# Kernel optimization log

Measured on AMD Instinct MI355X. Metric: run time of the kernel, lower is better.

## Reference

```python
import jax, jax.numpy as jnp
import numpy as np

B, L, E, H = 4, 2048, 512, 8
D = E // H
FACTOR = 5
U = min(FACTOR * int(np.ceil(np.log(L))), L)  # sample_k == n_top == 40


def setup_inputs() -> dict:
    key0 = jax.random.key(0)
    ks = jax.random.split(key0, 12)
    s = 0.02
    inp = {
        "query": jax.random.normal(ks[0], (B, L, E), jnp.float32),
        "key": jax.random.normal(ks[1], (B, L, E), jnp.float32),
        "value": jax.random.normal(ks[2], (B, L, E), jnp.float32),
        "index_sample": jax.random.randint(ks[3], (L, U), 0, L, jnp.int32),
    }
    for i, nm in enumerate(["q", "k", "v", "o"]):
        inp[f"W{nm}"] = jax.random.normal(ks[4 + i], (E, E), jnp.float32) * s
        inp[f"b{nm}"] = jnp.zeros((E,), jnp.float32)
    return inp


def reference(query, key, value, index_sample, Wq, bq, Wk, bk, Wv, bv, Wo, bo):
    # projections (nn.Linear: x @ W.T + b)
    q = (query @ Wq.T + bq).reshape(B, L, H, D).transpose(0, 2, 1, 3)  # [B,H,L,D]
    k = (key @ Wk.T + bk).reshape(B, L, H, D).transpose(0, 2, 1, 3)
    v = (value @ Wv.T + bv).reshape(B, L, H, D).transpose(0, 2, 1, 3)

    L_Q = L_K = L
    sample_k = index_sample.shape[1]
    n_top = min(sample_k, L_Q)

    # --- _prob_QK: sampled QK scores, note: NO 1/sqrt(D) scaling in source ---
    K_sample = k[:, :, index_sample, :]                      # [B,H,L_Q,sample_k,D]
    QK_sample = jnp.einsum('bhld,bhlsd->bhls', q, K_sample)  # [B,H,L_Q,sample_k]
    M = QK_sample.max(axis=-1) - QK_sample.sum(axis=-1) / L_K
    _, M_top = jax.lax.top_k(M, n_top)                       # [B,H,n_top]
    Q_reduce = jnp.take_along_axis(q, M_top[..., None], axis=2)  # [B,H,n_top,D]
    scores = jnp.einsum('bhud,bhkd->bhuk', Q_reduce, k)      # [B,H,n_top,L_K]

    # --- initial context (eval mode: mean of V) ---
    context = jnp.broadcast_to(v.mean(axis=2, keepdims=True), (B, H, L_Q, D))

    # --- update context at selected queries ---
    attn = jax.nn.softmax(scores, axis=-1)
    upd = jnp.einsum('bhuk,bhkd->bhud', attn, v)             # [B,H,n_top,D]
    bi = jnp.arange(B)[:, None, None]
    hi = jnp.arange(H)[None, :, None]
    context = context.at[bi, hi, M_top].set(upd)

    out = context.transpose(0, 2, 1, 3).reshape(B, L, E) @ Wo.T + bo
    return out
```

## Files before the change

kernel.cpp:

```cpp
#include <hip/hip_runtime.h>
#include <hip/hip_bf16.h>
#include <math.h>

constexpr int BB = 4;
constexpr int LL = 2048;
constexpr int EE = 512;
constexpr int HH = 8;
constexpr int DD = 64;
constexpr int UU = 40;
constexpr int NT = 40;
constexpr int NCH = 32;
constexpr int CK = 64;
constexpr int MVC = 16;
constexpr float NEG_INF = -3.0e38f;

typedef __attribute__((ext_vector_type(8))) short bf8_t;
typedef __attribute__((ext_vector_type(4))) float f4_t;

__device__ __forceinline__ void split2(float x, uint& h, uint& m)
{
    uint  xb = __float_as_uint(x);
    uint  hb = (xb + 0x7fffu + ((xb >> 16) & 1u)) & 0xffff0000u;
    float r  = x - __uint_as_float(hb);
    h = hb >> 16;
    m = (__float_as_uint(r) & 0xffff0000u) >> 16;
}

__device__ __forceinline__ int swz(int row, int c)
{
    return row * 64 + (((c ^ row ^ (row >> 2)) & 3) << 4);
}

__global__ __launch_bounds__(256, 4) void proj_kernel(
    const float* __restrict__ Xq, const float* __restrict__ Xk, const float* __restrict__ Xv,
    const float* __restrict__ Wq, const float* __restrict__ Wk, const float* __restrict__ Wv,
    const float* __restrict__ bq, const float* __restrict__ bk, const float* __restrict__ bv,
    float* __restrict__ Oq, float* __restrict__ Ok, float* __restrict__ Ov)
{
    const float* X; const float* W; const float* bias; float* O;
    if (blockIdx.z == 0)      { X = Xq; W = Wq; bias = bq; O = Oq; }
    else if (blockIdx.z == 1) { X = Xk; W = Wk; bias = bk; O = Ok; }
    else                      { X = Xv; W = Wv; bias = bv; O = Ov; }

    __shared__ char ldsmem[32768];
    char* const LA = ldsmem;
    char* const LB = ldsmem + 16384;

    const int tid  = threadIdx.x;
    const int lane = tid & 63;
    const int wave = tid >> 6;
    const int m0 = blockIdx.y * 128;
    const int n0 = blockIdx.x * 128;

    const int srow  = tid >> 1;
    const int shalf = tid & 1;
    const int w0 = swz(srow, shalf * 2);
    const int w1 = swz(srow, shalf * 2 + 1);
    const float* Aptr = X + (size_t)(m0 + srow) * EE + shalf * 16;
    const float* Bptr = W + (size_t)(n0 + srow) * EE + shalf * 16;

    const int rxor = ((((lane >> 4) ^ lane ^ (lane >> 2)) & 3) << 4);
    const int arow = (wave >> 1) * 64 + (lane & 15);
    const int brow = (wave & 1) * 64 + (lane & 15);

    f4_t acc[4][4];
#pragma unroll
    for (int i = 0; i < 4; i++)
#pragma unroll
        for (int j = 0; j < 4; j++) acc[i][j] = (f4_t)0.0f;

    for (int kt = 0; kt < EE; kt += 32) {
        float fa[16], fb[16];
#pragma unroll
        for (int q = 0; q < 4; q++) {
            *(float4*)(fa + q * 4) = *(const float4*)(Aptr + kt + q * 4);
            *(float4*)(fb + q * 4) = *(const float4*)(Bptr + kt + q * 4);
        }
        uint ahu[8], amu[8], bhu[8], bmu[8];
#pragma unroll
        for (int p = 0; p < 8; p++) {
            uint h0, m0_, h1, m1_;
            split2(fa[2 * p], h0, m0_);
            split2(fa[2 * p + 1], h1, m1_);
            ahu[p] = h0 | (h1 << 16); amu[p] = m0_ | (m1_ << 16);
            split2(fb[2 * p], h0, m0_);
            split2(fb[2 * p + 1], h1, m1_);
            bhu[p] = h0 | (h1 << 16); bmu[p] = m0_ | (m1_ << 16);
        }
        __syncthreads();
        *(uint4*)(LA +     0 + w0) = make_uint4(ahu[0], ahu[1], ahu[2], ahu[3]);
        *(uint4*)(LA +     0 + w1) = make_uint4(ahu[4], ahu[5], ahu[6], ahu[7]);
        *(uint4*)(LA +  8192 + w0) = make_uint4(amu[0], amu[1], amu[2], amu[3]);
        *(uint4*)(LA +  8192 + w1) = make_uint4(amu[4], amu[5], amu[6], amu[7]);
        *(uint4*)(LB +     0 + w0) = make_uint4(bhu[0], bhu[1], bhu[2], bhu[3]);
        *(uint4*)(LB +     0 + w1) = make_uint4(bhu[4], bhu[5], bhu[6], bhu[7]);
        *(uint4*)(LB +  8192 + w0) = make_uint4(bmu[0], bmu[1], bmu[2], bmu[3]);
        *(uint4*)(LB +  8192 + w1) = make_uint4(bmu[4], bmu[5], bmu[6], bmu[7]);
        __syncthreads();

        bf8_t af[4][2];
#pragma unroll
        for (int i = 0; i < 4; i++) {
            const int ro = (arow + i * 16) * 64 + rxor;
            af[i][0] = *(const bf8_t*)(LA +    0 + ro);
            af[i][1] = *(const bf8_t*)(LA + 8192 + ro);
        }
#pragma unroll
        for (int j = 0; j < 4; j++) {
            const int ro = (brow + j * 16) * 64 + rxor;
            bf8_t bh_ = *(const bf8_t*)(LB +    0 + ro);
            bf8_t bm_ = *(const bf8_t*)(LB + 8192 + ro);
#pragma unroll
            for (int i = 0; i < 4; i++) {
                f4_t c = acc[i][j];
                c = __builtin_amdgcn_mfma_f32_16x16x32_bf16(af[i][0], bh_, c, 0, 0, 0);
                c = __builtin_amdgcn_mfma_f32_16x16x32_bf16(af[i][0], bm_, c, 0, 0, 0);
                c = __builtin_amdgcn_mfma_f32_16x16x32_bf16(af[i][1], bh_, c, 0, 0, 0);
                acc[i][j] = c;
            }
        }
    }

#pragma unroll
    for (int j = 0; j < 4; j++) {
        const int n  = n0 + (wave & 1) * 64 + j * 16 + (lane & 15);
        const float bn = bias[n];
        const int h_ = n >> 6, d_ = n & 63;
#pragma unroll
        for (int i = 0; i < 4; i++) {
            const int mb = m0 + (wave >> 1) * 64 + i * 16 + ((lane >> 4) << 2);
#pragma unroll
            for (int r = 0; r < 4; r++) {
                const int m  = mb + r;
                const int b_ = m >> 11;
                const int l_ = m & (LL - 1);
                O[(((size_t)(b_ * HH + h_) * LL + l_) << 6) + d_] = acc[i][j][r] + bn;
            }
        }
    }
}

__global__ __launch_bounds__(256) void meanv_part_kernel(const float* __restrict__ v,
                                                         float* __restrict__ vpart)
{
    const int bh    = blockIdx.x & 31;
    const int chunk = blockIdx.x >> 5;
    const int d  = threadIdx.x & 63;
    const int wv = threadIdx.x >> 6;
    const float* base = v + ((size_t)bh * LL + chunk * 128 + wv * 32) * DD + d;
    float acc = 0.0f;
#pragma unroll
    for (int i = 0; i < 32; i++) acc += base[i * DD];
    __shared__ float red[4][DD];
    red[wv][d] = acc;
    __syncthreads();
    if (wv == 0)
        vpart[(size_t)(chunk * 32 + bh) * DD + d]
            = red[0][d] + red[1][d] + red[2][d] + red[3][d];
}

__global__ __launch_bounds__(64) void meanv_comb_kernel(const float* __restrict__ vpart,
                                                        float* __restrict__ mean_v)
{
    const int bh = blockIdx.x;
    const int d  = threadIdx.x;
    float s = 0.0f;
#pragma unroll
    for (int c = 0; c < MVC; c++) s += vpart[(size_t)(c * 32 + bh) * DD + d];
    mean_v[bh * DD + d] = s * (1.0f / (float)LL);
}

__global__ __launch_bounds__(256) void measure_kernel(const float* __restrict__ q,
                                                      const float* __restrict__ k,
                                                      const int* __restrict__ idx_sample,
                                                      float* __restrict__ M)
{
    int bh   = blockIdx.x & 31;
    int lc   = blockIdx.x >> 5;
    int lane = threadIdx.x & 63;
    int wv   = threadIdx.x >> 6;
    int l    = lc * 4 + wv;
    int s8   = lane >> 3;
    int c    = lane & 7;

    const float* qrow = q + ((size_t)bh * LL + l) * DD + c * 8;
    float4 q0 = *(const float4*)(qrow);
    float4 q1 = *(const float4*)(qrow + 4);

    const float* kbase = k + (size_t)bh * LL * DD;
    const int*   irow  = idx_sample + l * UU;

    float mx = NEG_INF, sum = 0.0f;
#pragma unroll
    for (int it = 0; it < UU; it += 8) {
        int ki = irow[it + s8];
        const float* krow = kbase + (size_t)ki * DD + c * 8;
        float4 k0 = *(const float4*)(krow);
        float4 k1 = *(const float4*)(krow + 4);
        float p = q0.x*k0.x + q0.y*k0.y + q0.z*k0.z + q0.w*k0.w
                + q1.x*k1.x + q1.y*k1.y + q1.z*k1.z + q1.w*k1.w;
        p += __shfl_xor(p, 1, 64);
        p += __shfl_xor(p, 2, 64);
        p += __shfl_xor(p, 4, 64);
        mx = fmaxf(mx, p);
        sum += p;
    }
    mx  = fmaxf(mx, __shfl_xor(mx, 8, 64));
    sum += __shfl_xor(sum, 8, 64);
    mx  = fmaxf(mx, __shfl_xor(mx, 16, 64));
    sum += __shfl_xor(sum, 16, 64);
    mx  = fmaxf(mx, __shfl_xor(mx, 32, 64));
    sum += __shfl_xor(sum, 32, 64);

    if (lane == 0) M[bh * LL + l] = mx - sum * (1.0f / (float)LL);
}

__global__ __launch_bounds__(64) void topk_kernel(const float* __restrict__ M,
                                                  int* __restrict__ top)
{
    const int bh   = blockIdx.x;
    const int lane = threadIdx.x;

    unsigned long long keys[32];
#pragma unroll
    for (int i = 0; i < 32; i++) {
        int idx = i * 64 + lane;
        uint u  = __float_as_uint(M[bh * LL + idx]);
        uint sv = (u & 0x80000000u) ? ~u : (u | 0x80000000u);
        keys[i] = ((unsigned long long)sv << 32) | (uint)(LL - 1 - idx);
    }
    unsigned long long lmax = 0ull;
#pragma unroll
    for (int i = 0; i < 32; i++) lmax = (keys[i] > lmax) ? keys[i] : lmax;

    for (int it = 0; it < NT; it++) {
        unsigned long long g = lmax;
#pragma unroll
        for (int off = 1; off < 64; off <<= 1) {
            unsigned long long o = __shfl_xor(g, off, 64);
            g = (o > g) ? o : g;
        }
        if (lane == 0) top[bh * NT + it] = LL - 1 - (int)(g & 0xffffffffu);
#pragma unroll
        for (int i = 0; i < 32; i++) if (keys[i] == g) keys[i] = 0ull;
        lmax = 0ull;
#pragma unroll
        for (int i = 0; i < 32; i++) lmax = (keys[i] > lmax) ? keys[i] : lmax;
    }
}

__global__ __launch_bounds__(256) void pv_kernel(const float* __restrict__ q,
                                                 const float* __restrict__ k,
                                                 const float* __restrict__ v,
                                                 const int* __restrict__ top,
                                                 float* __restrict__ mpart,
                                                 float* __restrict__ lpart,
                                                 float* __restrict__ accpart)
{
    const int bh    = blockIdx.x & 31;
    const int chunk = blockIdx.x >> 5;
    const int tid   = threadIdx.x;
    const int lane  = tid & 63, wv = tid >> 6;

    __shared__ float qs[NT][DD];
    __shared__ float sc[NT][CK + 4];

    for (int i = tid; i < NT * DD / 4; i += 256) {
        int u  = i >> 4;
        int d4 = (i & 15) * 4;
        int l  = top[bh * NT + u];
        *(float4*)&qs[u][d4] = *(const float4*)(q + ((size_t)bh * LL + l) * DD + d4);
    }
    __syncthreads();

    {
        const int key  = tid >> 2;
        const int dseg = tid & 3;
        const float* krow = k + ((size_t)bh * LL + chunk * CK + key) * DD + dseg * 16;
        float4 k0 = *(const float4*)(krow);
        float4 k1 = *(const float4*)(krow + 4);
        float4 k2 = *(const float4*)(krow + 8);
        float4 k3 = *(const float4*)(krow + 12);
#pragma unroll 8
        for (int u = 0; u < NT; u++) {
            const float* qrow = &qs[u][dseg * 16];
            float4 q0 = *(const float4*)(qrow);
            float4 q1 = *(const float4*)(qrow + 4);
            float4 q2 = *(const float4*)(qrow + 8);
            float4 q3 = *(const float4*)(qrow + 12);
            float p = k0.x*q0.x + k0.y*q0.y + k0.z*q0.z + k0.w*q0.w
                    + k1.x*q1.x + k1.y*q1.y + k1.z*q1.z + k1.w*q1.w
                    + k2.x*q2.x + k2.y*q2.y + k2.z*q2.z + k2.w*q2.w
                    + k3.x*q3.x + k3.y*q3.y + k3.z*q3.z + k3.w*q3.w;
            p += __shfl_xor(p, 1, 64);
            p += __shfl_xor(p, 2, 64);
            if (dseg == 0) sc[u][key] = p;
        }
    }
    __syncthreads();

#pragma unroll
    for (int i = 0; i < 10; i++) {
        const int u = wv * 10 + i;
        float val = sc[u][lane];
        float mx = val;
        mx = fmaxf(mx, __shfl_xor(mx, 1, 64));
        mx = fmaxf(mx, __shfl_xor(mx, 2, 64));
        mx = fmaxf(mx, __shfl_xor(mx, 4, 64));
        mx = fmaxf(mx, __shfl_xor(mx, 8, 64));
        mx = fmaxf(mx, __shfl_xor(mx, 16, 64));
        mx = fmaxf(mx, __shfl_xor(mx, 32, 64));
        float e = __expf(val - mx);
        sc[u][lane] = e;
        float s = e;
        s += __shfl_xor(s, 1, 64);
        s += __shfl_xor(s, 2, 64);
        s += __shfl_xor(s, 4, 64);
        s += __shfl_xor(s, 8, 64);
        s += __shfl_xor(s, 16, 64);
        s += __shfl_xor(s, 32, 64);
        if (lane == 0) {
            mpart[(bh * NCH + chunk) * NT + u] = mx;
            lpart[(bh * NCH + chunk) * NT + u] = s;
        }
    }
    __syncthreads();

    {
        float pacc[10];
#pragma unroll
        for (int i = 0; i < 10; i++) pacc[i] = 0.0f;
        const float* vbase = v + ((size_t)bh * LL + chunk * CK) * DD;
#pragma unroll 8
        for (int t = 0; t < CK; t++) {
            float vval = vbase[(size_t)t * DD + lane];
#pragma unroll
            for (int i = 0; i < 10; i++) pacc[i] += sc[wv * 10 + i][t] * vval;
        }
#pragma unroll
        for (int i = 0; i < 10; i++) {
            const int u = wv * 10 + i;
            accpart[(((size_t)(bh * NCH + chunk)) * NT + u) * 64 + lane] = pacc[i];
        }
    }
}

__global__ __launch_bounds__(256) void base_kernel(const float* __restrict__ mean_v,
                                                   const float* __restrict__ Wo,
                                                   const float* __restrict__ bo,
                                                   float* __restrict__ base)
{
    int lane = threadIdx.x & 63, wv = threadIdx.x >> 6;
    int be = blockIdx.x * 4 + wv;
    int b  = be >> 9;
    int e  = be & (EE - 1);
    const float* mrow = mean_v + b * EE;
    const float* wrow = Wo + (size_t)e * EE;
    float acc = 0.0f;
#pragma unroll
    for (int j = 0; j < 8; j++) acc += mrow[lane + j * 64] * wrow[lane + j * 64];
#pragma unroll
    for (int off = 32; off > 0; off >>= 1) acc += __shfl_down(acc, off, 64);
    if (lane == 0) base[be] = acc + bo[e];
}

__global__ __launch_bounds__(256) void bcast_kernel(const float* __restrict__ base,
                                                    float* __restrict__ out)
{
    size_t fi = ((size_t)blockIdx.x * 256 + threadIdx.x) * 4;
    int b  = (int)(fi >> 20);
    int e4 = (int)(fi & (EE - 1));
    float4 val = *(const float4*)(base + b * EE + e4);
    *(float4*)(out + fi) = val;
}

__global__ __launch_bounds__(256) void corr_kernel(const float* __restrict__ accpart,
                                                   const float* __restrict__ lpart,
                                                   const float* __restrict__ mpart,
                                                   const float* __restrict__ mean_v,
                                                   const int* __restrict__ top,
                                                   const float* __restrict__ Wo,
                                                   float* __restrict__ out)
{
    int bhu = blockIdx.x;
    int bh  = bhu / NT;
    int u   = bhu % NT;
    int h   = bh & (HH - 1);
    int b   = bh >> 3;
    int tid = threadIdx.x;
    int l   = top[bhu];

    __shared__ float delta[DD];
    if (tid < DD) {
        float m = NEG_INF;
#pragma unroll 8
        for (int c = 0; c < NCH; c++) m = fmaxf(m, mpart[(bh * NCH + c) * NT + u]);
        float den = 0.0f, num = 0.0f;
#pragma unroll 8
        for (int c = 0; c < NCH; c++) {
            float f = __expf(mpart[(bh * NCH + c) * NT + u] - m);
            den += lpart[(bh * NCH + c) * NT + u] * f;
            num += accpart[(((size_t)(bh * NCH + c)) * NT + u) * 64 + tid] * f;
        }
        delta[tid] = num / den - mean_v[bh * DD + tid];
    }
    __syncthreads();

    float* orow = out + ((size_t)(b * LL + l)) * EE;
#pragma unroll
    for (int rep = 0; rep < 2; rep++) {
        int e = tid + rep * 256;
        const float* wrow = Wo + (size_t)e * EE + h * DD;
        float acc = 0.0f;
#pragma unroll
        for (int d = 0; d < DD; d++) acc += delta[d] * wrow[d];
        atomicAdd(orow + e, acc);
    }
}

extern "C" void kernel_launch(void* const* d_in, const int* in_sizes, int n_in,
                              void* d_out, int out_size, void* d_ws, size_t ws_size,
                              hipStream_t stream)
{
    const float* query = (const float*)d_in[0];
    const float* key   = (const float*)d_in[1];
    const float* value = (const float*)d_in[2];
    const int*   idxs  = (const int*)d_in[3];
    const float* Wq = (const float*)d_in[4];
    const float* bq = (const float*)d_in[5];
    const float* Wk = (const float*)d_in[6];
    const float* bk = (const float*)d_in[7];
    const float* Wv = (const float*)d_in[8];
    const float* bv = (const float*)d_in[9];
    const float* Wo = (const float*)d_in[10];
    const float* bo = (const float*)d_in[11];
    float* out = (float*)d_out;

    char* ws = (char*)d_ws;
    size_t off = 0;
    const size_t qkv_bytes = (size_t)BB * HH * LL * DD * sizeof(float);
    float* q_ws = (float*)(ws + off); off += qkv_bytes;
    float* k_ws = (float*)(ws + off); off += qkv_bytes;
    float* v_ws = (float*)(ws + off); off += qkv_bytes;
    float* M_ws    = (float*)(ws + off); off += (size_t)BB * HH * LL * sizeof(float);
    int*   top_ws  = (int*)(ws + off);   off += (size_t)BB * HH * NT * sizeof(int);
    float* mean_ws = (float*)(ws + off); off += (size_t)BB * HH * DD * sizeof(float);
    float* vpart_ws = (float*)(ws + off); off += (size_t)BB * HH * MVC * DD * sizeof(float);
    float* mpart_ws = (float*)(ws + off); off += (size_t)BB * HH * NCH * NT * sizeof(float);
    float* lpart_ws = (float*)(ws + off); off += (size_t)BB * HH * NCH * NT * sizeof(float);
    float* accpart_ws = (float*)(ws + off); off += (size_t)BB * HH * NCH * NT * DD * sizeof(float);
    float* base_ws = (float*)(ws + off); off += (size_t)BB * EE * sizeof(float);

    dim3 g1(EE / 128, (BB * LL) / 128, 3);
    proj_kernel<<<g1, 256, 0, stream>>>(query, key, value, Wq, Wk, Wv, bq, bk, bv,
                                        q_ws, k_ws, v_ws);
    meanv_part_kernel<<<BB * HH * MVC, 256, 0, stream>>>(v_ws, vpart_ws);
    meanv_comb_kernel<<<BB * HH, 64, 0, stream>>>(vpart_ws, mean_ws);
    measure_kernel<<<(LL / 4) * 32, 256, 0, stream>>>(q_ws, k_ws, idxs, M_ws);
    topk_kernel<<<BB * HH, 64, 0, stream>>>(M_ws, top_ws);
    pv_kernel<<<BB * HH * NCH, 256, 0, stream>>>(q_ws, k_ws, v_ws, top_ws,
                                                 mpart_ws, lpart_ws, accpart_ws);
    base_kernel<<<(BB * EE) / 4, 256, 0, stream>>>(mean_ws, Wo, bo, base_ws);
    bcast_kernel<<<(BB * LL * EE) / (256 * 4), 256, 0, stream>>>(base_ws, out);
    corr_kernel<<<BB * HH * NT, 256, 0, stream>>>(accpart_ws, lpart_ws, mpart_ws,
                                                  mean_ws, top_ws, Wo, out);
}
```

Measured before the change: 312.1 us.

## Pre-split weights to bf16 pairs, async-load B tiles into LDS with double buffering

A new kernel converts Wq/Wk/Wv into high and residual bf16 halves once per call. The projection GEMM then streams those halves straight into a double-buffered LDS region with global_load_lds, and prefetches the next A slice into registers, instead of reloading and splitting fp32 W in every tile. The grid is remapped to a 1D XCD-aware ordering, and occupancy is lowered to allow 48KB LDS. The pv kernel is also changed to read 4 scores at a time as float4 from LDS. The converted weights reuse the accpart workspace before pv_kernel writes it, which is safe only because of stream ordering.

```diff
diff --git a/kernel.cpp b/kernel.cpp
--- a/kernel.cpp
+++ b/kernel.cpp
@@ -26,38 +26,93 @@
     m = (__float_as_uint(r) & 0xffff0000u) >> 16;
 }
 
+__device__ __forceinline__ void split2pair(float x0, float x1, uint& hp, uint& mp)
+{
+    uint xb0 = __float_as_uint(x0), xb1 = __float_as_uint(x1);
+    uint hb0 = xb0 + 0x7fffu + ((xb0 >> 16) & 1u);
+    uint hb1 = xb1 + 0x7fffu + ((xb1 >> 16) & 1u);
+    hp = __builtin_amdgcn_perm(hb1, hb0, 0x07060302u);
+    float r0 = x0 - __uint_as_float(hb0 & 0xffff0000u);
+    float r1 = x1 - __uint_as_float(hb1 & 0xffff0000u);
+    mp = __builtin_amdgcn_perm(__float_as_uint(r1), __float_as_uint(r0), 0x07060302u);
+}
+
+__device__ __forceinline__ void gload16(const void* g, void* l)
+{
+    __builtin_amdgcn_global_load_lds(
+        (const __attribute__((address_space(1))) unsigned int*)g,
+        (__attribute__((address_space(3))) unsigned int*)l, 16, 0, 0);
+}
+
 __device__ __forceinline__ int swz(int row, int c)
 {
     return row * 64 + (((c ^ row ^ (row >> 2)) & 3) << 4);
 }
 
-__global__ __launch_bounds__(256, 4) void proj_kernel(
+__global__ __launch_bounds__(256) void wconv_kernel(
+    const float* __restrict__ Wq, const float* __restrict__ Wk,
+    const float* __restrict__ Wv, unsigned short* __restrict__ wcv)
+{
+    const int gi  = blockIdx.x * 256 + threadIdx.x;
+    const int z   = gi >> 15;
+    const int off = (gi & 32767) * 8;
+    const float* W = (z == 0) ? Wq : (z == 1 ? Wk : Wv);
+    float x[8];
+    *(float4*)(x)     = *(const float4*)(W + off);
+    *(float4*)(x + 4) = *(const float4*)(W + off + 4);
+    uint hp[4], mp[4];
+#pragma unroll
+    for (int p = 0; p < 4; p++) split2pair(x[2 * p], x[2 * p + 1], hp[p], mp[p]);
+    unsigned short* Wh = wcv + (size_t)z * 524288;
+    *(uint4*)(Wh + off)          = make_uint4(hp[0], hp[1], hp[2], hp[3]);
+    *(uint4*)(Wh + 262144 + off) = make_uint4(mp[0], mp[1], mp[2], mp[3]);
+}
+
+__global__ __launch_bounds__(256, 3) void proj_kernel(
     const float* __restrict__ Xq, const float* __restrict__ Xk, const float* __restrict__ Xv,
-    const float* __restrict__ Wq, const float* __restrict__ Wk, const float* __restrict__ Wv,
+    const unsigned short* __restrict__ Wcv,
     const float* __restrict__ bq, const float* __restrict__ bk, const float* __restrict__ bv,
     float* __restrict__ Oq, float* __restrict__ Ok, float* __restrict__ Ov)
 {
-    const float* X; const float* W; const float* bias; float* O;
-    if (blockIdx.z == 0)      { X = Xq; W = Wq; bias = bq; O = Oq; }
-    else if (blockIdx.z == 1) { X = Xk; W = Wk; bias = bk; O = Ok; }
-    else                      { X = Xv; W = Wv; bias = bv; O = Ov; }
-
-    __shared__ char ldsmem[32768];
+    const int bid = blockIdx.x;
+    const int xg  = bid & 7;
+    const int s   = bid >> 3;
+    const int yz  = xg * 24 + (s >> 2);
+    const int zi  = yz >> 6;
+    const int yi  = yz & 63;
+    const int m0  = yi * 128;
+    const int n0  = (s & 3) * 128;
+
+    const float* X; const float* bias; float* O;
+    if (zi == 0)      { X = Xq; bias = bq; O = Oq; }
+    else if (zi == 1) { X = Xk; bias = bk; O = Ok; }
+    else              { X = Xv; bias = bv; O = Ov; }
+    const unsigned short* Wh = Wcv + (size_t)zi * 524288;
+    const unsigned short* Wm = Wh + 262144;
+
+    __shared__ char ldsmem[49152];
     char* const LA = ldsmem;
     char* const LB = ldsmem + 16384;
 
     const int tid  = threadIdx.x;
     const int lane = tid & 63;
     const int wave = tid >> 6;
-    const int m0 = blockIdx.y * 128;
-    const int n0 = blockIdx.x * 128;
 
     const int srow  = tid >> 1;
     const int shalf = tid & 1;
     const int w0 = swz(srow, shalf * 2);
     const int w1 = swz(srow, shalf * 2 + 1);
     const float* Aptr = X + (size_t)(m0 + srow) * EE + shalf * 16;
-    const float* Bptr = W + (size_t)(n0 + srow) * EE + shalf * 16;
+
+    const int r0 = tid >> 2;
+    const int r1 = 64 + r0;
+    const int c0 = (tid & 3) ^ ((r0 ^ (r0 >> 2)) & 3);
+    const int c1 = (tid & 3) ^ ((r1 ^ (r1 >> 2)) & 3);
+    const unsigned short* bh0 = Wh + (size_t)(n0 + r0) * EE + c0 * 8;
+    const unsigned short* bh1 = Wh + (size_t)(n0 + r1) * EE + c1 * 8;
+    const unsigned short* bm0 = Wm + (size_t)(n0 + r0) * EE + c0 * 8;
+    const unsigned short* bm1 = Wm + (size_t)(n0 + r1) * EE + c1 * 8;
+    const int ldst = tid * 16;
 
     const int rxor = ((((lane >> 4) ^ lane ^ (lane >> 2)) & 3) << 4);
     const int arow = (wave >> 1) * 64 + (lane & 15);
@@ -69,35 +124,43 @@
 #pragma unroll
         for (int j = 0; j < 4; j++) acc[i][j] = (f4_t)0.0f;
 
+    float fa[16];
+#pragma unroll
+    for (int q = 0; q < 4; q++)
+        *(float4*)(fa + q * 4) = *(const float4*)(Aptr + q * 4);
+    gload16(bh0, LB + ldst);
+    gload16(bh1, LB + 4096 + ldst);
+    gload16(bm0, LB + 8192 + ldst);
+    gload16(bm1, LB + 12288 + ldst);
+
+    int parity = 0;
+#pragma unroll 2
     for (int kt = 0; kt < EE; kt += 32) {
-        float fa[16], fb[16];
-#pragma unroll
-        for (int q = 0; q < 4; q++) {
-            *(float4*)(fa + q * 4) = *(const float4*)(Aptr + kt + q * 4);
-            *(float4*)(fb + q * 4) = *(const float4*)(Bptr + kt + q * 4);
-        }
-        uint ahu[8], amu[8], bhu[8], bmu[8];
-#pragma unroll
-        for (int p = 0; p < 8; p++) {
-            uint h0, m0_, h1, m1_;
-            split2(fa[2 * p], h0, m0_);
-            split2(fa[2 * p + 1], h1, m1_);
-            ahu[p] = h0 | (h1 << 16); amu[p] = m0_ | (m1_ << 16);
-            split2(fb[2 * p], h0, m0_);
-            split2(fb[2 * p + 1], h1, m1_);
-            bhu[p] = h0 | (h1 << 16); bmu[p] = m0_ | (m1_ << 16);
-        }
+        uint ahu[8], amu[8];
+#pragma unroll
+        for (int p = 0; p < 8; p++)
+            split2pair(fa[2 * p], fa[2 * p + 1], ahu[p], amu[p]);
+
         __syncthreads();
-        *(uint4*)(LA +     0 + w0) = make_uint4(ahu[0], ahu[1], ahu[2], ahu[3]);
-        *(uint4*)(LA +     0 + w1) = make_uint4(ahu[4], ahu[5], ahu[6], ahu[7]);
-        *(uint4*)(LA +  8192 + w0) = make_uint4(amu[0], amu[1], amu[2], amu[3]);
-        *(uint4*)(LA +  8192 + w1) = make_uint4(amu[4], amu[5], amu[6], amu[7]);
-        *(uint4*)(LB +     0 + w0) = make_uint4(bhu[0], bhu[1], bhu[2], bhu[3]);
-        *(uint4*)(LB +     0 + w1) = make_uint4(bhu[4], bhu[5], bhu[6], bhu[7]);
-        *(uint4*)(LB +  8192 + w0) = make_uint4(bmu[0], bmu[1], bmu[2], bmu[3]);
-        *(uint4*)(LB +  8192 + w1) = make_uint4(bmu[4], bmu[5], bmu[6], bmu[7]);
+        *(uint4*)(LA +    0 + w0) = make_uint4(ahu[0], ahu[1], ahu[2], ahu[3]);
+        *(uint4*)(LA +    0 + w1) = make_uint4(ahu[4], ahu[5], ahu[6], ahu[7]);
+        *(uint4*)(LA + 8192 + w0) = make_uint4(amu[0], amu[1], amu[2], amu[3]);
+        *(uint4*)(LA + 8192 + w1) = make_uint4(amu[4], amu[5], amu[6], amu[7]);
         __syncthreads();
 
+        if (kt + 32 < EE) {
+            const int kn = kt + 32;
+#pragma unroll
+            for (int q = 0; q < 4; q++)
+                *(float4*)(fa + q * 4) = *(const float4*)(Aptr + kn + q * 4);
+            char* Bn = LB + (parity ^ 1) * 16384;
+            gload16(bh0 + kn, Bn + ldst);
+            gload16(bh1 + kn, Bn + 4096 + ldst);
+            gload16(bm0 + kn, Bn + 8192 + ldst);
+            gload16(bm1 + kn, Bn + 12288 + ldst);
+        }
+
+        char* const Bb = LB + parity * 16384;
         bf8_t af[4][2];
 #pragma unroll
         for (int i = 0; i < 4; i++) {
@@ -108,8 +171,8 @@
 #pragma unroll
         for (int j = 0; j < 4; j++) {
             const int ro = (brow + j * 16) * 64 + rxor;
-            bf8_t bh_ = *(const bf8_t*)(LB +    0 + ro);
-            bf8_t bm_ = *(const bf8_t*)(LB + 8192 + ro);
+            bf8_t bh_ = *(const bf8_t*)(Bb +    0 + ro);
+            bf8_t bm_ = *(const bf8_t*)(Bb + 8192 + ro);
 #pragma unroll
             for (int i = 0; i < 4; i++) {
                 f4_t c = acc[i][j];
@@ -119,6 +182,7 @@
                 acc[i][j] = c;
             }
         }
+        parity ^= 1;
     }
 
 #pragma unroll
@@ -262,8 +326,8 @@
     const int tid   = threadIdx.x;
     const int lane  = tid & 63, wv = tid >> 6;
 
-    __shared__ float qs[NT][DD];
-    __shared__ float sc[NT][CK + 4];
+    __shared__ alignas(16) float qs[NT][DD];
+    __shared__ alignas(16) float sc[NT][CK + 4];
 
     for (int i = tid; i < NT * DD / 4; i += 256) {
         int u  = i >> 4;
@@ -330,12 +394,18 @@
         float pacc[10];
 #pragma unroll
         for (int i = 0; i < 10; i++) pacc[i] = 0.0f;
-        const float* vbase = v + ((size_t)bh * LL + chunk * CK) * DD;
-#pragma unroll 8
-        for (int t = 0; t < CK; t++) {
-            float vval = vbase[(size_t)t * DD + lane];
-#pragma unroll
-            for (int i = 0; i < 10; i++) pacc[i] += sc[wv * 10 + i][t] * vval;
+        const float* vbase = v + ((size_t)bh * LL + chunk * CK) * DD + lane;
+#pragma unroll 4
+        for (int t = 0; t < CK; t += 4) {
+            float v0 = vbase[(size_t)(t + 0) * DD];
+            float v1 = vbase[(size_t)(t + 1) * DD];
+            float v2 = vbase[(size_t)(t + 2) * DD];
+            float v3 = vbase[(size_t)(t + 3) * DD];
+#pragma unroll
+            for (int i = 0; i < 10; i++) {
+                float4 s = *(const float4*)&sc[wv * 10 + i][t];
+                pacc[i] += s.x * v0 + s.y * v1 + s.z * v2 + s.w * v3;
+            }
         }
 #pragma unroll
         for (int i = 0; i < 10; i++) {
@@ -451,9 +521,11 @@
     float* accpart_ws = (float*)(ws + off); off += (size_t)BB * HH * NCH * NT * DD * sizeof(float);
     float* base_ws = (float*)(ws + off); off += (size_t)BB * EE * sizeof(float);
 
-    dim3 g1(EE / 128, (BB * LL) / 128, 3);
-    proj_kernel<<<g1, 256, 0, stream>>>(query, key, value, Wq, Wk, Wv, bq, bk, bv,
-                                        q_ws, k_ws, v_ws);
+    unsigned short* wcv_ws = (unsigned short*)accpart_ws;
+
+    wconv_kernel<<<384, 256, 0, stream>>>(Wq, Wk, Wv, wcv_ws);
+    proj_kernel<<<768, 256, 0, stream>>>(query, key, value, wcv_ws, bq, bk, bv,
+                                         q_ws, k_ws, v_ws);
     meanv_part_kernel<<<BB * HH * MVC, 256, 0, stream>>>(v_ws, vpart_ws);
     meanv_comb_kernel<<<BB * HH, 64, 0, stream>>>(vpart_ws, mean_ws);
     measure_kernel<<<(LL / 4) * 32, 256, 0, stream>>>(q_ws, k_ws, idxs, M_ws);
```

Result: no change. 316.3 us (+1.4%).
